# Kernel optimization log

Hardware: AMD Instinct MI355X
Metric: run time of the kernel (lower is better)

Reference implementation:

```python
import jax, jax.numpy as jnp
import numpy as np

NUM_UNITS = 64
IN_FEATURES = 256
OUT_FEATURES = 256


def _uw(x, w):
    # per-unit linear: x [B,U,I], w [U,I,O] -> [B,U,O]
    return jnp.einsum('bui,uio->buo', x, w)


def setup_inputs() -> dict:
    key = jax.random.key(0)
    ks = jax.random.split(key, 8)
    bound = float(np.sqrt(1.0 / OUT_FEATURES))
    U, I, O = NUM_UNITS, IN_FEATURES, OUT_FEATURES
    B = 256
    uni = lambda k, s: jax.random.uniform(k, s, jnp.float32, -bound, bound)
    return {
        'x': jax.random.normal(ks[0], (B, U, I), jnp.float32),
        'w_ir': uni(ks[1], (U, I, O)),
        'w_iz': uni(ks[2], (U, I, O)),
        'w_in': uni(ks[3], (U, I, O)),
        'w_hr': uni(ks[4], (U, O, O)),
        'w_hz': uni(ks[5], (U, O, O)),
        'w_hn': uni(ks[6], (U, O, O)),
        'hidden_init': uni(ks[7], (1, U, O)),
    }


def reference(x, w_ir, w_iz, w_in, w_hr, w_hz, w_hn, hidden_init):
    # hidden initialized by broadcasting hidden_init over batch (first call)
    h = jnp.broadcast_to(hidden_init, (x.shape[0],) + hidden_init.shape[1:])
    r = jax.nn.sigmoid(_uw(x, w_ir) + _uw(h, w_hr))
    z = jax.nn.sigmoid(_uw(x, w_iz) + _uw(h, w_hz))
    n = jnp.tanh(_uw(x, w_in) + r * _uw(h, w_hn))
    return (1.0 - z) * n + z * h
```

## Files before the change

### kernel.cpp

```cpp
#include <hip/hip_runtime.h>

#define BATCH 256
#define UNITS 64
#define IFEAT 256
#define OFEAT 256

typedef __attribute__((ext_vector_type(8))) short v8s;
typedef __attribute__((ext_vector_type(4))) float v4f;

static __device__ __forceinline__ unsigned short f2bf(float f) {
    unsigned int x = __float_as_uint(f);
    unsigned int r = x + 0x7fffu + ((x >> 16) & 1u);
    return (unsigned short)(r >> 16);
}

static __device__ __forceinline__ float sigmoid_f(float x) {
    return 1.0f / (1.0f + __expf(-x));
}
static __device__ __forceinline__ float tanh_f(float x) {
    float ax = fabsf(x);
    float e = __expf(-2.0f * ax);
    float t = (1.0f - e) / (1.0f + e);
    return copysignf(t, x);
}

__global__ __launch_bounds__(512, 8) void gru_hvec(
        const float* __restrict__ whr,
        const float* __restrict__ whz,
        const float* __restrict__ whn,
        const float* __restrict__ hinit,
        float* __restrict__ hv) {
    __shared__ float red[512];
    const int bid  = blockIdx.x;
    const int half = bid & 1;
    const int u    = (bid >> 1) & 63;
    const int w    = bid >> 7;
    const float* wh = (w == 0) ? whr : (w == 1) ? whz : whn;

    const int t = threadIdx.x;
    const int o = half * 128 + (t & 127);
    const int c = t >> 7;
    const float* hp = hinit + u * IFEAT;
    const float* wp = wh + (size_t)u * IFEAT * OFEAT + o;

    float acc = 0.0f;
    const int i0 = c * 64;
#pragma unroll 8
    for (int i = 0; i < 64; ++i) {
        acc += hp[i0 + i] * wp[(size_t)(i0 + i) * OFEAT];
    }
    red[t] = acc;
    __syncthreads();
    if (c == 0)
        hv[((size_t)w * UNITS + u) * OFEAT + o] =
            red[t] + red[t + 128] + red[t + 256] + red[t + 384];
}

__global__ __launch_bounds__(256, 2) void gru_gemm(
    const float* __restrict__ x,
    const float* __restrict__ wir,
    const float* __restrict__ wiz,
    const float* __restrict__ win,
    const float* __restrict__ hinit,
    const float* __restrict__ hv,
    float* __restrict__ out) {
    __shared__ unsigned short As[32][64][8];
    __shared__ unsigned short Bs[3][32][32][8];

    const int bid = blockIdx.x;
    const int idx = bid >> 3;
    const int u   = (bid & 7) * 8 + (idx >> 5);
    const int rem = idx & 31;
    const int b0  = (rem >> 3) * 64;
    const int o0  = (rem & 7) * 32;

    const int t    = threadIdx.x;
    const int lane = t & 63;
    const int wave = t >> 6;
    const int wm   = wave >> 1;
    const int wn   = wave & 1;
    const int lg   = lane >> 4;
    const int lr   = lane & 15;

#pragma unroll
    for (int c = 0; c < 12; ++c) {
        const int id  = c * 256 + t;
        const int col = id & 31;
        const int kq  = (id >> 5) & 31;
        const int g   = id >> 10;
        const float* wp = (g == 0) ? wir : (g == 1) ? wiz : win;
        const int off = u * (IFEAT * OFEAT) + (kq * 8) * OFEAT + o0 + col;
        float rb[8];
#pragma unroll
        for (int j = 0; j < 8; ++j) rb[j] = wp[off + j * OFEAT];
        v8s bv;
#pragma unroll
        for (int j = 0; j < 8; ++j) bv[j] = (short)f2bf(rb[j]);
        *(v8s*)&Bs[g][kq][col][0] = bv;
    }

    {
        const int kq   = t & 31;
        const int rsub = t >> 5;
#pragma unroll
        for (int c = 0; c < 8; ++c) {
            const int row = c * 8 + rsub;
            const float* ap = x + (b0 + row) * (UNITS * IFEAT) + u * IFEAT + kq * 8;
            v4f q0 = *(const v4f*)ap;
            v4f q1 = *(const v4f*)(ap + 4);
            v8s av;
            av[0] = (short)f2bf(q0[0]); av[1] = (short)f2bf(q0[1]);
            av[2] = (short)f2bf(q0[2]); av[3] = (short)f2bf(q0[3]);
            av[4] = (short)f2bf(q1[0]); av[5] = (short)f2bf(q1[1]);
            av[6] = (short)f2bf(q1[2]); av[7] = (short)f2bf(q1[3]);
            *(v8s*)&As[kq][(row + kq) & 63][0] = av;
        }
    }

    __syncthreads();

    v4f acc[3][2];
#pragma unroll
    for (int g = 0; g < 3; ++g)
#pragma unroll
        for (int mi = 0; mi < 2; ++mi)
            acc[g][mi] = (v4f){0.f, 0.f, 0.f, 0.f};

#pragma unroll
    for (int kk = 0; kk < 8; ++kk) {
        const int kq0 = kk * 4 + lg;
        v8s a0 = *(const v8s*)&As[kq0][((wm * 32 + lr) + kq0) & 63][0];
        v8s a1 = *(const v8s*)&As[kq0][((wm * 32 + 16 + lr) + kq0) & 63][0];
#pragma unroll
        for (int g = 0; g < 3; ++g) {
            v8s b = *(const v8s*)&Bs[g][kq0][wn * 16 + lr][0];
            acc[g][0] = __builtin_amdgcn_mfma_f32_16x16x32_bf16(a0, b, acc[g][0], 0, 0, 0);
            acc[g][1] = __builtin_amdgcn_mfma_f32_16x16x32_bf16(a1, b, acc[g][1], 0, 0, 0);
        }
    }

    const int o = o0 + wn * 16 + lr;
    const float hrv = hv[(0 * UNITS + u) * OFEAT + o];
    const float hzv = hv[(1 * UNITS + u) * OFEAT + o];
    const float hnv = hv[(2 * UNITS + u) * OFEAT + o];
    const float h0v = hinit[u * OFEAT + o];
    const int rbase = b0 + wm * 32 + lg * 4;
#pragma unroll
    for (int mi = 0; mi < 2; ++mi) {
#pragma unroll
        for (int jj = 0; jj < 4; ++jj) {
            const int row = rbase + mi * 16 + jj;
            const float r = sigmoid_f(acc[0][mi][jj] + hrv);
            const float z = sigmoid_f(acc[1][mi][jj] + hzv);
            const float n = tanh_f(acc[2][mi][jj] + r * hnv);
            out[(row * UNITS + u) * OFEAT + o] = (1.0f - z) * n + z * h0v;
        }
    }
}

extern "C" void kernel_launch(void* const* d_in, const int* in_sizes, int n_in,
                              void* d_out, int out_size, void* d_ws, size_t ws_size,
                              hipStream_t stream) {
    const float* x     = (const float*)d_in[0];
    const float* w_ir  = (const float*)d_in[1];
    const float* w_iz  = (const float*)d_in[2];
    const float* w_in  = (const float*)d_in[3];
    const float* w_hr  = (const float*)d_in[4];
    const float* w_hz  = (const float*)d_in[5];
    const float* w_hn  = (const float*)d_in[6];
    const float* hinit = (const float*)d_in[7];
    float* out = (float*)d_out;
    float* hv  = (float*)d_ws;

    gru_hvec<<<dim3(384), dim3(512), 0, stream>>>(w_hr, w_hz, w_hn, hinit, hv);
    gru_gemm<<<dim3(2048), dim3(256), 0, stream>>>(x, w_ir, w_iz, w_in, hinit, hv, out);
}
```

Baseline: 37.25 us.

## Double block threads, coalesce x loads, pipeline weight loads, use hardware bf16 packing

The GEMM block grows from 256 to 512 threads (8 waves), and each wave now computes a 16x16 tile per gate instead of 32x16, so there is more parallelism per block and fewer accumulators per thread. The x tile is loaded with coalesced float4 reads into registers before the weight loads are issued. Weight loads are software-pipelined across two register buffers so global latency overlaps the bf16 conversion and LDS stores. Manual bf16 rounding is replaced with the packed __float22bfloat162_rn intrinsic. The cost is fewer blocks resident per CU and a different LDS write pattern for A that may cause bank conflicts.

```diff
diff --git a/kernel.cpp b/kernel.cpp
--- a/kernel.cpp
+++ b/kernel.cpp
@@ -1,4 +1,5 @@
 #include <hip/hip_runtime.h>
+#include <hip/hip_bf16.h>
 
 #define BATCH 256
 #define UNITS 64
@@ -8,10 +9,10 @@
 typedef __attribute__((ext_vector_type(8))) short v8s;
 typedef __attribute__((ext_vector_type(4))) float v4f;
 
-static __device__ __forceinline__ unsigned short f2bf(float f) {
-    unsigned int x = __float_as_uint(f);
-    unsigned int r = x + 0x7fffu + ((x >> 16) & 1u);
-    return (unsigned short)(r >> 16);
+static __device__ __forceinline__ unsigned int pk2(float a, float b) {
+    union { __hip_bfloat162 h; unsigned int u; } c;
+    c.h = __float22bfloat162_rn(float2{a, b});
+    return c.u;
 }
 
 static __device__ __forceinline__ float sigmoid_f(float x) {
@@ -56,7 +57,7 @@
             red[t] + red[t + 128] + red[t + 256] + red[t + 384];
 }
 
-__global__ __launch_bounds__(256, 2) void gru_gemm(
+__global__ __launch_bounds__(512, 4) void gru_gemm(
     const float* __restrict__ x,
     const float* __restrict__ wir,
     const float* __restrict__ wiz,
@@ -76,66 +77,84 @@
 
     const int t    = threadIdx.x;
     const int lane = t & 63;
-    const int wave = t >> 6;
-    const int wm   = wave >> 1;
-    const int wn   = wave & 1;
+    const int wv   = t >> 6;
+    const int wm   = wv >> 1;
+    const int wn   = wv & 1;
     const int lg   = lane >> 4;
     const int lr   = lane & 15;
 
+    v4f areg[8];
 #pragma unroll
-    for (int c = 0; c < 12; ++c) {
-        const int id  = c * 256 + t;
-        const int col = id & 31;
-        const int kq  = (id >> 5) & 31;
-        const int g   = id >> 10;
-        const float* wp = (g == 0) ? wir : (g == 1) ? wiz : win;
-        const int off = u * (IFEAT * OFEAT) + (kq * 8) * OFEAT + o0 + col;
-        float rb[8];
-#pragma unroll
-        for (int j = 0; j < 8; ++j) rb[j] = wp[off + j * OFEAT];
-        v8s bv;
-#pragma unroll
-        for (int j = 0; j < 8; ++j) bv[j] = (short)f2bf(rb[j]);
-        *(v8s*)&Bs[g][kq][col][0] = bv;
+    for (int i = 0; i < 8; ++i) {
+        const int row = wv * 8 + i;
+        areg[i] = *(const v4f*)(x + (size_t)(b0 + row) * (UNITS * IFEAT)
+                                  + u * IFEAT + lane * 4);
     }
 
+    const int bcol = t & 31;
+    const int bkqh = t >> 5;
+    float rbA[8], rbB[8];
+
+    auto bload = [&](int c, float* rb) {
+        const int g  = c >> 1;
+        const int kq = (c & 1) * 16 + bkqh;
+        const float* wp = (g == 0) ? wir : (g == 1) ? wiz : win;
+        const float* p = wp + (size_t)u * (IFEAT * OFEAT) + (kq * 8) * OFEAT + o0 + bcol;
+#pragma unroll
+        for (int j = 0; j < 8; ++j) rb[j] = p[j * OFEAT];
+    };
+    auto bstore = [&](int c, const float* rb) {
+        const int g  = c >> 1;
+        const int kq = (c & 1) * 16 + bkqh;
+        uint4 v;
+        v.x = pk2(rb[0], rb[1]);
+        v.y = pk2(rb[2], rb[3]);
+        v.z = pk2(rb[4], rb[5]);
+        v.w = pk2(rb[6], rb[7]);
+        *(uint4*)&Bs[g][kq][bcol][0] = v;
+    };
+
+    bload(0, rbA);
+    bload(1, rbB);
+    bstore(0, rbA);
+    bload(2, rbA);
+    bstore(1, rbB);
+    bload(3, rbB);
+    bstore(2, rbA);
+    bload(4, rbA);
+    bstore(3, rbB);
+    bload(5, rbB);
+    bstore(4, rbA);
+    bstore(5, rbB);
+
     {
-        const int kq   = t & 31;
-        const int rsub = t >> 5;
+        const int kqA = lane >> 1;
+        const int j0  = (lane & 1) * 4;
 #pragma unroll
-        for (int c = 0; c < 8; ++c) {
-            const int row = c * 8 + rsub;
-            const float* ap = x + (b0 + row) * (UNITS * IFEAT) + u * IFEAT + kq * 8;
-            v4f q0 = *(const v4f*)ap;
-            v4f q1 = *(const v4f*)(ap + 4);
-            v8s av;
-            av[0] = (short)f2bf(q0[0]); av[1] = (short)f2bf(q0[1]);
-            av[2] = (short)f2bf(q0[2]); av[3] = (short)f2bf(q0[3]);
-            av[4] = (short)f2bf(q1[0]); av[5] = (short)f2bf(q1[1]);
-            av[6] = (short)f2bf(q1[2]); av[7] = (short)f2bf(q1[3]);
-            *(v8s*)&As[kq][(row + kq) & 63][0] = av;
+        for (int i = 0; i < 8; ++i) {
+            const int row = wv * 8 + i;
+            const int rot = (row + kqA) & 63;
+            uint2 v;
+            v.x = pk2(areg[i][0], areg[i][1]);
+            v.y = pk2(areg[i][2], areg[i][3]);
+            *(uint2*)&As[kqA][rot][j0] = v;
         }
     }
 
     __syncthreads();
 
-    v4f acc[3][2];
+    v4f acc[3];
 #pragma unroll
-    for (int g = 0; g < 3; ++g)
-#pragma unroll
-        for (int mi = 0; mi < 2; ++mi)
-            acc[g][mi] = (v4f){0.f, 0.f, 0.f, 0.f};
+    for (int g = 0; g < 3; ++g) acc[g] = (v4f){0.f, 0.f, 0.f, 0.f};
 
 #pragma unroll
     for (int kk = 0; kk < 8; ++kk) {
         const int kq0 = kk * 4 + lg;
-        v8s a0 = *(const v8s*)&As[kq0][((wm * 32 + lr) + kq0) & 63][0];
-        v8s a1 = *(const v8s*)&As[kq0][((wm * 32 + 16 + lr) + kq0) & 63][0];
+        v8s a0 = *(const v8s*)&As[kq0][((wm * 16 + lr) + kq0) & 63][0];
 #pragma unroll
         for (int g = 0; g < 3; ++g) {
             v8s b = *(const v8s*)&Bs[g][kq0][wn * 16 + lr][0];
-            acc[g][0] = __builtin_amdgcn_mfma_f32_16x16x32_bf16(a0, b, acc[g][0], 0, 0, 0);
-            acc[g][1] = __builtin_amdgcn_mfma_f32_16x16x32_bf16(a1, b, acc[g][1], 0, 0, 0);
+            acc[g] = __builtin_amdgcn_mfma_f32_16x16x32_bf16(a0, b, acc[g], 0, 0, 0);
         }
     }
 
@@ -144,17 +163,14 @@
     const float hzv = hv[(1 * UNITS + u) * OFEAT + o];
     const float hnv = hv[(2 * UNITS + u) * OFEAT + o];
     const float h0v = hinit[u * OFEAT + o];
-    const int rbase = b0 + wm * 32 + lg * 4;
+    const int rbase = b0 + wm * 16 + lg * 4;
 #pragma unroll
-    for (int mi = 0; mi < 2; ++mi) {
-#pragma unroll
-        for (int jj = 0; jj < 4; ++jj) {
-            const int row = rbase + mi * 16 + jj;
-            const float r = sigmoid_f(acc[0][mi][jj] + hrv);
-            const float z = sigmoid_f(acc[1][mi][jj] + hzv);
-            const float n = tanh_f(acc[2][mi][jj] + r * hnv);
-            out[(row * UNITS + u) * OFEAT + o] = (1.0f - z) * n + z * h0v;
-        }
+    for (int jj = 0; jj < 4; ++jj) {
+        const int row = rbase + jj;
+        const float r = sigmoid_f(acc[0][jj] + hrv);
+        const float z = sigmoid_f(acc[1][jj] + hzv);
+        const float n = tanh_f(acc[2][jj] + r * hnv);
+        out[(row * UNITS + u) * OFEAT + o] = (1.0f - z) * n + z * h0v;
     }
 }
 
@@ -173,5 +189,5 @@
     float* hv  = (float*)d_ws;
 
     gru_hvec<<<dim3(384), dim3(512), 0, stream>>>(w_hr, w_hz, w_hn, hinit, hv);
-    gru_gemm<<<dim3(2048), dim3(256), 0, stream>>>(x, w_ir, w_iz, w_in, hinit, hv, out);
+    gru_gemm<<<dim3(2048), dim3(512), 0, stream>>>(x, w_ir, w_iz, w_in, hinit, hv, out);
 }
```

Result: no change. 37.34 us (+0.2%).
